# Kernel tuning notes

Measured on AMD Instinct MI355X. Metric: run time of the kernel, lower is better.

Reference implementation:

```python
import jax, jax.numpy as jnp
import numpy as np

N_NODES = 20000
N_EDGES = 8192
UNITS = 128
NUM_GAUSSIANS = 50
CUTOFF = 8.0
GAMMA = 10.0
MIN_DIST, MAX_DIST = 0.0, 30.0


def setup_inputs() -> dict:
    key = jax.random.key(0)
    ks = jax.random.split(key, 6)
    node_features = jax.random.normal(ks[0], (N_NODES, UNITS), dtype=jnp.float32)
    edge_indices = jax.random.randint(ks[1], (2, N_EDGES), 0, N_NODES, dtype=jnp.int32)
    distances = jax.random.uniform(ks[2], (N_EDGES,), dtype=jnp.float32)
    # filter network params (Dense(units) -> swish -> Dense(units*units))
    W1 = jax.random.normal(ks[3], (NUM_GAUSSIANS, UNITS), dtype=jnp.float32) / np.sqrt(NUM_GAUSSIANS)
    b1 = jnp.zeros((UNITS,), dtype=jnp.float32)
    W2 = jax.random.normal(ks[4], (UNITS, UNITS * UNITS), dtype=jnp.float32) / np.sqrt(UNITS)
    b2 = jnp.zeros((UNITS * UNITS,), dtype=jnp.float32)
    # transform Dense(units, use_bias=False)
    Wt = jax.random.normal(ks[5], (UNITS, UNITS), dtype=jnp.float32) / np.sqrt(UNITS)
    return {"node_features": node_features, "edge_indices": edge_indices,
            "distances": distances, "W1": W1, "b1": b1, "W2": W2, "b2": b2, "Wt": Wt}


def reference(node_features, edge_indices, distances, W1, b1, W2, b2, Wt):
    n_nodes, units = node_features.shape
    # cutoff mask (multiplicative; dropped edges contribute zero to the scatter-sum,
    # equivalent to tf.boolean_mask + unsorted_segment_sum)
    mask = (distances <= CUTOFF).astype(node_features.dtype)  # [E]
    # Gaussian basis expansion
    centers = jnp.linspace(MIN_DIST, MAX_DIST, NUM_GAUSSIANS, dtype=jnp.float32)
    df = jnp.exp(-GAMMA * jnp.square(distances[:, None] - centers[None, :]))  # [E, G]
    # filter network: Dense -> swish -> Dense(units*units)
    h = jax.nn.silu(df @ W1 + b1)                    # [E, U]
    filters = (h @ W2 + b2).reshape(-1, units, units)  # [E, U, U]
    # gather source node features, transform, per-edge matvec
    src = node_features[edge_indices[0]]             # [E, U]
    transformed = src @ Wt                           # [E, U]
    filtered = jnp.einsum('eij,ej->ei', filters, transformed) * mask[:, None]  # [E, U]
    # scatter-sum to destination nodes
    messages = jax.ops.segment_sum(filtered, edge_indices[1], num_segments=n_nodes)
    return jax.nn.silu(messages)
```

## Files before the change

kernel.cpp:

```cpp
#include <hip/hip_runtime.h>
#include <hip/hip_fp16.h>


typedef _Float16 f16;
typedef __attribute__((ext_vector_type(8))) f16 f16x8;
typedef __attribute__((ext_vector_type(4))) float f32x4;
typedef __attribute__((ext_vector_type(4))) unsigned int u32x4;

#define NEDGE 8192
#define NNODE 20000
#define NG    50
#define KSTEPS 516
#define W2C_BYTES (KSTEPS * 8192)
#define HT_BYTES (64 * 132 * 128 * 2)
#define TM_BYTES (NEDGE * 128 * 2)

#define LDS_H   0
#define LDS_TM  5120
#define LDS_TOT 37888

static __device__ __forceinline__ float fsilu(float x) { return x / (1.0f + __expf(-x)); }

static __device__ __forceinline__ void gll16(const void* g, void* l) {
  __builtin_amdgcn_global_load_lds(
      (const __attribute__((address_space(1))) unsigned int*)g,
      (__attribute__((address_space(3))) unsigned int*)l, 16, 0, 0);
}

__global__ __launch_bounds__(256) void k0_w2c(const float* __restrict__ W2,
                                              const float* __restrict__ b2,
                                              f16* __restrict__ w2c) {
  int gidx = blockIdx.x * 256 + threadIdx.x;
  int lane = gidx & 63;
  int nt   = (gidx >> 6) & 7;
  int step = gidx >> 9;
  int k0i = step * 32 + (lane >> 4) * 8;
  int i   = nt * 16 + (lane & 15);
  int u   = k0i >> 7, j0 = k0i & 127;
  const float* src = (u < 128) ? (W2 + (size_t)u * 16384 + i * 128 + j0)
                               : (b2 + i * 128 + j0);
  union { f16 s[8]; u32x4 v; } pk;
#pragma unroll
  for (int r = 0; r < 8; ++r) pk.s[r] = (f16)src[r];
  *((u32x4*)w2c + gidx) = pk.v;
}

__global__ __launch_bounds__(256) void k1_edge(const float* __restrict__ NF,
                                               const int*   __restrict__ EI,
                                               const float* __restrict__ DI,
                                               const float* __restrict__ W1,
                                               const float* __restrict__ B1,
                                               const float* __restrict__ WT,
                                               f16* __restrict__ ht2,
                                               f16* __restrict__ tmo) {
  __shared__ float df[16][NG];
  __shared__ float s_mask[16];
  __shared__ float s_src[16][128];
  __shared__ float t_tile[16][132];
  __shared__ float h_tile[16][132];
  int et = blockIdx.x, e0 = et * 16, tid = threadIdx.x;

  for (int idx = tid; idx < 16 * NG; idx += 256) {
    int e = idx / NG, g = idx - e * NG;
    float d = DI[e0 + e];
    float x = d - (float)g * (30.0f / 49.0f);
    df[e][g] = __expf(-10.0f * x * x);
  }
  if (tid < 16) s_mask[tid] = (DI[e0 + tid] <= 8.0f) ? 1.0f : 0.0f;
  for (int idx = tid; idx < 16 * 128; idx += 256) {
    int e = idx >> 7, u = idx & 127;
    s_src[e][u] = NF[(size_t)EI[e0 + e] * 128 + u];
  }
  __syncthreads();

  int j = tid & 127, es = tid >> 7;
  for (int e = es * 8; e < es * 8 + 8; ++e) {
    float acc = B1[j];
    for (int g = 0; g < NG; ++g) acc += df[e][g] * W1[g * 128 + j];
    h_tile[e][j] = fsilu(acc);
  }
  {
    float acc[8] = {0.f,0.f,0.f,0.f,0.f,0.f,0.f,0.f};
    for (int u = 0; u < 128; ++u) {
      float wv = WT[u * 128 + j];
#pragma unroll
      for (int e8 = 0; e8 < 8; ++e8) acc[e8] += s_src[es * 8 + e8][u] * wv;
    }
#pragma unroll
    for (int e8 = 0; e8 < 8; ++e8) t_tile[es * 8 + e8][j] = acc[e8];
  }
  __syncthreads();

  int eb = et >> 3, el0 = (et & 7) * 16;
  {
    int u = tid >> 1, hf = tid & 1;
    union { f16 s[8]; u32x4 v; } pk;
#pragma unroll
    for (int k = 0; k < 8; ++k) pk.s[k] = (f16)h_tile[hf * 8 + k][u];
    *(u32x4*)(ht2 + ((size_t)eb * 132 + u) * 128 + el0 + hf * 8) = pk.v;
  }
  if (tid < 16) ht2[((size_t)eb * 132 + 128) * 128 + el0 + tid] = (f16)1.0f;
  {
    int e = tid >> 4, cc = tid & 15;
    float m = s_mask[e];
    union { f16 s[8]; u32x4 v; } pk;
#pragma unroll
    for (int k = 0; k < 8; ++k) pk.s[k] = (f16)(m * t_tile[e][cc * 8 + k]);
    int col = (cc * 16) ^ ((e & 7) << 4);
    *(u32x4*)((char*)tmo + (size_t)(e0 + e) * 256 + col) = pk.v;
  }
}

__global__ __launch_bounds__(256, 2) void k2_gemm(const f16* __restrict__ w2c,
                                                  const f16* __restrict__ ht2,
                                                  const f16* __restrict__ tm,
                                                  const int* __restrict__ EI,
                                                  float* __restrict__ msg) {
  __shared__ u32x4 smem_v[LDS_TOT / 16];
  char* smem = (char*)smem_v;

  const int bid = blockIdx.x;
  const int c   = bid & 7;
  const int eb  = bid >> 3;
  const int e0  = eb * 128;
  const int nu  = (c == 7) ? 17 : 16;
  const int tid = threadIdx.x, w = tid >> 6, lane = tid & 63;
  const int l15 = lane & 15, g4 = lane >> 4;
  const int wm = w >> 1, wn = w & 1;

  {
    const char* tsrc = (const char*)tm + (size_t)e0 * 256 + w * 8192;
#pragma unroll
    for (int q = 0; q < 8; ++q)
      gll16(tsrc + q * 1024 + lane * 16,
            smem + LDS_TM + w * 8192 + q * 1024 + lane * 16);
  }
  if (w == 0) {
    const char* hsrc = (const char*)ht2 + ((size_t)eb * 132 + c * 16) * 256;
#pragma unroll
    for (int q = 0; q < 5; ++q)
      gll16(hsrc + q * 1024 + lane * 16, smem + LDS_H + q * 1024 + lane * 16);
  }
  __syncthreads();

  f16x8 Tall[4][4];
  {
    const int tmrow = LDS_TM + (wm * 64 + l15) * 256;
    const int colsw = (l15 & 7) << 4;
#pragma unroll
    for (int rt = 0; rt < 4; ++rt)
#pragma unroll
      for (int jc = 0; jc < 4; ++jc)
        Tall[rt][jc] = *(const f16x8*)(smem + tmrow + rt * 4096 +
                                       ((jc * 64 + g4 * 16) ^ colsw));
  }
  const __half* hbase = (const __half*)(smem + LDS_H) + wm * 64 + l15;

  __half2 hc[4], hn[4];
#pragma unroll
  for (int rt = 0; rt < 4; ++rt) hc[rt] = __half2half2(hbase[rt * 16]);

  const char* bp = (const char*)w2c + (size_t)(c * 64) * 8192 + wn * 4096 + lane * 16;
  f16x8 Bc[4], Bn[4];
#pragma unroll
  for (int nt = 0; nt < 4; ++nt) Bn[nt] = *(const f16x8*)(bp + nt * 1024);
  bp += 8192;

  f32x4 acc[4][4];
#pragma unroll
  for (int rt = 0; rt < 4; ++rt)
#pragma unroll
    for (int nt = 0; nt < 4; ++nt) acc[rt][nt] = (f32x4){0.f, 0.f, 0.f, 0.f};

  for (int u = 0; u < nu; ++u) {
#pragma unroll
    for (int jc = 0; jc < 4; ++jc) {
#pragma unroll
      for (int nt = 0; nt < 4; ++nt) Bc[nt] = Bn[nt];
#pragma unroll
      for (int nt = 0; nt < 4; ++nt) Bn[nt] = *(const f16x8*)(bp + nt * 1024);
      bp += 8192;
      if (jc == 1) {
#pragma unroll
        for (int rt = 0; rt < 4; ++rt)
          hn[rt] = __half2half2(hbase[(u + 1) * 128 + rt * 16]);
      }
      union uf { f16x8 v; __half2 h[4]; };
      uf a[4];
#pragma unroll
      for (int rt = 0; rt < 4; ++rt) {
        uf t; t.v = Tall[rt][jc];
#pragma unroll
        for (int q = 0; q < 4; ++q) a[rt].h[q] = __hmul2(t.h[q], hc[rt]);
      }
      __builtin_amdgcn_s_setprio(1);
#pragma unroll
      for (int nt = 0; nt < 4; ++nt)
#pragma unroll
        for (int rt = 0; rt < 4; ++rt)
          acc[rt][nt] = __builtin_amdgcn_mfma_f32_16x16x32_f16(a[rt].v, Bc[nt], acc[rt][nt], 0, 0, 0);
      __builtin_amdgcn_s_setprio(0);
    }
#pragma unroll
    for (int rt = 0; rt < 4; ++rt) hc[rt] = hn[rt];
  }

  const int* dst = EI + NEDGE;
#pragma unroll
  for (int rt = 0; rt < 4; ++rt) {
#pragma unroll
    for (int r = 0; r < 4; ++r) {
      int e = e0 + wm * 64 + rt * 16 + g4 * 4 + r;
      float* row = msg + (size_t)dst[e] * 128 + wn * 64 + l15;
#pragma unroll
      for (int nt = 0; nt < 4; ++nt)
        atomicAdd(row + nt * 16, acc[rt][nt][r]);
    }
  }
}

__global__ __launch_bounds__(256) void k3_silu(float* __restrict__ out, int n4) {
  int idx = blockIdx.x * 256 + threadIdx.x;
  int stride = gridDim.x * 256;
  f32x4* p = (f32x4*)out;
  for (; idx < n4; idx += stride) {
    f32x4 v = p[idx];
#pragma unroll
    for (int cc = 0; cc < 4; ++cc) v[cc] = fsilu(v[cc]);
    p[idx] = v;
  }
}

extern "C" void kernel_launch(void* const* d_in, const int* in_sizes, int n_in,
                              void* d_out, int out_size, void* d_ws, size_t ws_size,
                              hipStream_t stream) {
  const float* NF = (const float*)d_in[0];
  const int*   EI = (const int*)  d_in[1];
  const float* DI = (const float*)d_in[2];
  const float* W1 = (const float*)d_in[3];
  const float* B1 = (const float*)d_in[4];
  const float* W2 = (const float*)d_in[5];
  const float* B2 = (const float*)d_in[6];
  const float* WT = (const float*)d_in[7];
  float* out = (float*)d_out;

  f16* w2c = (f16*)d_ws;
  f16* ht2 = (f16*)((char*)d_ws + W2C_BYTES);
  f16* tmo = (f16*)((char*)d_ws + W2C_BYTES + HT_BYTES);
  size_t needed = (size_t)W2C_BYTES + HT_BYTES + TM_BYTES;
  if (ws_size < needed) return;

  hipMemsetAsync(d_out, 0, (size_t)out_size * sizeof(float), stream);
  k0_w2c <<<dim3(1032), dim3(256), 0, stream>>>(W2, B2, w2c);
  k1_edge<<<dim3(512),  dim3(256), 0, stream>>>(NF, EI, DI, W1, B1, WT, ht2, tmo);
  k2_gemm<<<dim3(512),  dim3(256), 0, stream>>>(w2c, ht2, tmo, EI, out);
  k3_silu<<<dim3(1024), dim3(256), 0, stream>>>(out, out_size / 4);
}
```

Baseline: 89.63 us.

## Fuse weight conversion, edge prep and zeroing; split GEMM across eight waves

The W2 f16 conversion, the per-edge filter and transform prep, and the output zeroing now run as block ranges of one kernel, replacing three separate launches including a memset. The edge GEMM kernel moves from 256 to 512 threads, so each wave owns 32 edge rows instead of 64. This halves the per-wave accumulator and A-operand registers and raises the number of resident waves. In exchange, each W2 B-fragment is now fetched from global memory by twice as many waves, which adds cache traffic.

Result: slower. 91.99 us (+2.6%).

```diff
diff --git a/kernel.cpp b/kernel.cpp
--- a/kernel.cpp
+++ b/kernel.cpp
@@ -27,91 +27,106 @@
       (__attribute__((address_space(3))) unsigned int*)l, 16, 0, 0);
 }
 
-__global__ __launch_bounds__(256) void k0_w2c(const float* __restrict__ W2,
-                                              const float* __restrict__ b2,
-                                              f16* __restrict__ w2c) {
-  int gidx = blockIdx.x * 256 + threadIdx.x;
-  int lane = gidx & 63;
-  int nt   = (gidx >> 6) & 7;
-  int step = gidx >> 9;
-  int k0i = step * 32 + (lane >> 4) * 8;
-  int i   = nt * 16 + (lane & 15);
-  int u   = k0i >> 7, j0 = k0i & 127;
-  const float* src = (u < 128) ? (W2 + (size_t)u * 16384 + i * 128 + j0)
-                               : (b2 + i * 128 + j0);
-  union { f16 s[8]; u32x4 v; } pk;
-#pragma unroll
-  for (int r = 0; r < 8; ++r) pk.s[r] = (f16)src[r];
-  *((u32x4*)w2c + gidx) = pk.v;
-}
-
-__global__ __launch_bounds__(256) void k1_edge(const float* __restrict__ NF,
-                                               const int*   __restrict__ EI,
-                                               const float* __restrict__ DI,
-                                               const float* __restrict__ W1,
-                                               const float* __restrict__ B1,
-                                               const float* __restrict__ WT,
-                                               f16* __restrict__ ht2,
-                                               f16* __restrict__ tmo) {
+__global__ __launch_bounds__(256) void k01(const float* __restrict__ W2,
+                                           const float* __restrict__ b2,
+                                           const float* __restrict__ NF,
+                                           const int*   __restrict__ EI,
+                                           const float* __restrict__ DI,
+                                           const float* __restrict__ W1,
+                                           const float* __restrict__ B1,
+                                           const float* __restrict__ WT,
+                                           f16* __restrict__ w2c,
+                                           f16* __restrict__ ht2,
+                                           f16* __restrict__ tmo,
+                                           float* __restrict__ out, int nz4) {
   __shared__ float df[16][NG];
   __shared__ float s_mask[16];
   __shared__ float s_src[16][128];
   __shared__ float t_tile[16][132];
   __shared__ float h_tile[16][132];
-  int et = blockIdx.x, e0 = et * 16, tid = threadIdx.x;
-
-  for (int idx = tid; idx < 16 * NG; idx += 256) {
-    int e = idx / NG, g = idx - e * NG;
-    float d = DI[e0 + e];
-    float x = d - (float)g * (30.0f / 49.0f);
-    df[e][g] = __expf(-10.0f * x * x);
-  }
-  if (tid < 16) s_mask[tid] = (DI[e0 + tid] <= 8.0f) ? 1.0f : 0.0f;
-  for (int idx = tid; idx < 16 * 128; idx += 256) {
-    int e = idx >> 7, u = idx & 127;
-    s_src[e][u] = NF[(size_t)EI[e0 + e] * 128 + u];
-  }
-  __syncthreads();
-
-  int j = tid & 127, es = tid >> 7;
-  for (int e = es * 8; e < es * 8 + 8; ++e) {
-    float acc = B1[j];
-    for (int g = 0; g < NG; ++g) acc += df[e][g] * W1[g * 128 + j];
-    h_tile[e][j] = fsilu(acc);
+  const int bid = blockIdx.x, tid = threadIdx.x;
+
+  if (bid < 1032) {
+    int gidx = bid * 256 + tid;
+    int lane = gidx & 63;
+    int nt   = (gidx >> 6) & 7;
+    int step = gidx >> 9;
+    int k0i = step * 32 + (lane >> 4) * 8;
+    int i   = nt * 16 + (lane & 15);
+    int u   = k0i >> 7, j0 = k0i & 127;
+    const float* src = (u < 128) ? (W2 + (size_t)u * 16384 + i * 128 + j0)
+                                 : (b2 + i * 128 + j0);
+    union { f16 s[8]; u32x4 v; } pk;
+#pragma unroll
+    for (int r = 0; r < 8; ++r) pk.s[r] = (f16)src[r];
+    *((u32x4*)w2c + gidx) = pk.v;
+    return;
+  }
+  if (bid < 1544) {
+    int et = bid - 1032, e0 = et * 16;
+    for (int idx = tid; idx < 16 * NG; idx += 256) {
+      int e = idx / NG, g = idx - e * NG;
+      float d = DI[e0 + e];
+      float x = d - (float)g * (30.0f / 49.0f);
+      df[e][g] = __expf(-10.0f * x * x);
+    }
+    if (tid < 16) s_mask[tid] = (DI[e0 + tid] <= 8.0f) ? 1.0f : 0.0f;
+    for (int idx = tid; idx < 16 * 128; idx += 256) {
+      int e = idx >> 7, u = idx & 127;
+      s_src[e][u] = NF[(size_t)EI[e0 + e] * 128 + u];
+    }
+    __syncthreads();
+
+    int j = tid & 127, es = tid >> 7;
+    for (int e = es * 8; e < es * 8 + 8; ++e) {
+      float acc = B1[j];
+      for (int g = 0; g < NG; ++g) acc += df[e][g] * W1[g * 128 + j];
+      h_tile[e][j] = fsilu(acc);
+    }
+    {
+      float acc[8] = {0.f,0.f,0.f,0.f,0.f,0.f,0.f,0.f};
+      for (int u = 0; u < 128; ++u) {
+        float wv = WT[u * 128 + j];
+#pragma unroll
+        for (int e8 = 0; e8 < 8; ++e8) acc[e8] += s_src[es * 8 + e8][u] * wv;
+      }
+#pragma unroll
+      for (int e8 = 0; e8 < 8; ++e8) t_tile[es * 8 + e8][j] = acc[e8];
+    }
+    __syncthreads();
+
+    int eb = et >> 3, el0 = (et & 7) * 16;
+    {
+      int u = tid >> 1, hf = tid & 1;
+      union { f16 s[8]; u32x4 v; } pk;
+#pragma unroll
+      for (int k = 0; k < 8; ++k) pk.s[k] = (f16)h_tile[hf * 8 + k][u];
+      *(u32x4*)(ht2 + ((size_t)eb * 132 + u) * 128 + el0 + hf * 8) = pk.v;
+    }
+    if (tid < 16) ht2[((size_t)eb * 132 + 128) * 128 + el0 + tid] = (f16)1.0f;
+    {
+      int e = tid >> 4, cc = tid & 15;
+      float m = s_mask[e];
+      union { f16 s[8]; u32x4 v; } pk;
+#pragma unroll
+      for (int k = 0; k < 8; ++k) pk.s[k] = (f16)(m * t_tile[e][cc * 8 + k]);
+      int col = (cc * 16) ^ ((e & 7) << 4);
+      *(u32x4*)((char*)tmo + (size_t)(e0 + e) * 256 + col) = pk.v;
+    }
+    return;
   }
   {
-    float acc[8] = {0.f,0.f,0.f,0.f,0.f,0.f,0.f,0.f};
-    for (int u = 0; u < 128; ++u) {
-      float wv = WT[u * 128 + j];
-#pragma unroll
-      for (int e8 = 0; e8 < 8; ++e8) acc[e8] += s_src[es * 8 + e8][u] * wv;
-    }
-#pragma unroll
-    for (int e8 = 0; e8 < 8; ++e8) t_tile[es * 8 + e8][j] = acc[e8];
-  }
-  __syncthreads();
-
-  int eb = et >> 3, el0 = (et & 7) * 16;
-  {
-    int u = tid >> 1, hf = tid & 1;
-    union { f16 s[8]; u32x4 v; } pk;
-#pragma unroll
-    for (int k = 0; k < 8; ++k) pk.s[k] = (f16)h_tile[hf * 8 + k][u];
-    *(u32x4*)(ht2 + ((size_t)eb * 132 + u) * 128 + el0 + hf * 8) = pk.v;
-  }
-  if (tid < 16) ht2[((size_t)eb * 132 + 128) * 128 + el0 + tid] = (f16)1.0f;
-  {
-    int e = tid >> 4, cc = tid & 15;
-    float m = s_mask[e];
-    union { f16 s[8]; u32x4 v; } pk;
-#pragma unroll
-    for (int k = 0; k < 8; ++k) pk.s[k] = (f16)(m * t_tile[e][cc * 8 + k]);
-    int col = (cc * 16) ^ ((e & 7) << 4);
-    *(u32x4*)((char*)tmo + (size_t)(e0 + e) * 256 + col) = pk.v;
-  }
-}
-
-__global__ __launch_bounds__(256, 2) void k2_gemm(const f16* __restrict__ w2c,
+    int base = (bid - 1544) * 1024;
+    f32x4 z = {0.f, 0.f, 0.f, 0.f};
+#pragma unroll
+    for (int k = 0; k < 4; ++k) {
+      int i4 = base + k * 256 + tid;
+      if (i4 < nz4) ((f32x4*)out)[i4] = z;
+    }
+  }
+}
+
+__global__ __launch_bounds__(512, 4) void k2_gemm(const f16* __restrict__ w2c,
                                                   const f16* __restrict__ ht2,
                                                   const f16* __restrict__ tm,
                                                   const int* __restrict__ EI,
@@ -129,36 +144,35 @@
   const int wm = w >> 1, wn = w & 1;
 
   {
-    const char* tsrc = (const char*)tm + (size_t)e0 * 256 + w * 8192;
-#pragma unroll
-    for (int q = 0; q < 8; ++q)
-      gll16(tsrc + q * 1024 + lane * 16,
-            smem + LDS_TM + w * 8192 + q * 1024 + lane * 16);
-  }
-  if (w == 0) {
+    const char* tsrc = (const char*)tm + (size_t)e0 * 256;
+#pragma unroll
+    for (int q = 0; q < 4; ++q) {
+      int off = (q * 512 + tid) * 16;
+      gll16(tsrc + off, smem + LDS_TM + off);
+    }
+  }
+  if (tid < 320) {
     const char* hsrc = (const char*)ht2 + ((size_t)eb * 132 + c * 16) * 256;
-#pragma unroll
-    for (int q = 0; q < 5; ++q)
-      gll16(hsrc + q * 1024 + lane * 16, smem + LDS_H + q * 1024 + lane * 16);
+    gll16(hsrc + tid * 16, smem + LDS_H + tid * 16);
   }
   __syncthreads();
 
-  f16x8 Tall[4][4];
+  f16x8 Tall[2][4];
   {
-    const int tmrow = LDS_TM + (wm * 64 + l15) * 256;
+    const int tmrow = LDS_TM + (wm * 32 + l15) * 256;
     const int colsw = (l15 & 7) << 4;
 #pragma unroll
-    for (int rt = 0; rt < 4; ++rt)
+    for (int rt = 0; rt < 2; ++rt)
 #pragma unroll
       for (int jc = 0; jc < 4; ++jc)
         Tall[rt][jc] = *(const f16x8*)(smem + tmrow + rt * 4096 +
                                        ((jc * 64 + g4 * 16) ^ colsw));
   }
-  const __half* hbase = (const __half*)(smem + LDS_H) + wm * 64 + l15;
-
-  __half2 hc[4], hn[4];
-#pragma unroll
-  for (int rt = 0; rt < 4; ++rt) hc[rt] = __half2half2(hbase[rt * 16]);
+  const __half* hbase = (const __half*)(smem + LDS_H) + wm * 32 + l15;
+
+  __half2 hc[2], hn[2];
+#pragma unroll
+  for (int rt = 0; rt < 2; ++rt) hc[rt] = __half2half2(hbase[rt * 16]);
 
   const char* bp = (const char*)w2c + (size_t)(c * 64) * 8192 + wn * 4096 + lane * 16;
   f16x8 Bc[4], Bn[4];
@@ -166,9 +180,9 @@
   for (int nt = 0; nt < 4; ++nt) Bn[nt] = *(const f16x8*)(bp + nt * 1024);
   bp += 8192;
 
-  f32x4 acc[4][4];
-#pragma unroll
-  for (int rt = 0; rt < 4; ++rt)
+  f32x4 acc[2][4];
+#pragma unroll
+  for (int rt = 0; rt < 2; ++rt)
 #pragma unroll
     for (int nt = 0; nt < 4; ++nt) acc[rt][nt] = (f32x4){0.f, 0.f, 0.f, 0.f};
 
@@ -182,13 +196,13 @@
       bp += 8192;
       if (jc == 1) {
 #pragma unroll
-        for (int rt = 0; rt < 4; ++rt)
+        for (int rt = 0; rt < 2; ++rt)
           hn[rt] = __half2half2(hbase[(u + 1) * 128 + rt * 16]);
       }
       union uf { f16x8 v; __half2 h[4]; };
-      uf a[4];
-#pragma unroll
-      for (int rt = 0; rt < 4; ++rt) {
+      uf a[2];
+#pragma unroll
+      for (int rt = 0; rt < 2; ++rt) {
         uf t; t.v = Tall[rt][jc];
 #pragma unroll
         for (int q = 0; q < 4; ++q) a[rt].h[q] = __hmul2(t.h[q], hc[rt]);
@@ -197,20 +211,20 @@
 #pragma unroll
       for (int nt = 0; nt < 4; ++nt)
 #pragma unroll
-        for (int rt = 0; rt < 4; ++rt)
+        for (int rt = 0; rt < 2; ++rt)
           acc[rt][nt] = __builtin_amdgcn_mfma_f32_16x16x32_f16(a[rt].v, Bc[nt], acc[rt][nt], 0, 0, 0);
       __builtin_amdgcn_s_setprio(0);
     }
 #pragma unroll
-    for (int rt = 0; rt < 4; ++rt) hc[rt] = hn[rt];
+    for (int rt = 0; rt < 2; ++rt) hc[rt] = hn[rt];
   }
 
   const int* dst = EI + NEDGE;
 #pragma unroll
-  for (int rt = 0; rt < 4; ++rt) {
+  for (int rt = 0; rt < 2; ++rt) {
 #pragma unroll
     for (int r = 0; r < 4; ++r) {
-      int e = e0 + wm * 64 + rt * 16 + g4 * 4 + r;
+      int e = e0 + wm * 32 + rt * 16 + g4 * 4 + r;
       float* row = msg + (size_t)dst[e] * 128 + wn * 64 + l15;
 #pragma unroll
       for (int nt = 0; nt < 4; ++nt)
@@ -250,9 +264,10 @@
   size_t needed = (size_t)W2C_BYTES + HT_BYTES + TM_BYTES;
   if (ws_size < needed) return;
 
-  hipMemsetAsync(d_out, 0, (size_t)out_size * sizeof(float), stream);
-  k0_w2c <<<dim3(1032), dim3(256), 0, stream>>>(W2, B2, w2c);
-  k1_edge<<<dim3(512),  dim3(256), 0, stream>>>(NF, EI, DI, W1, B1, WT, ht2, tmo);
-  k2_gemm<<<dim3(512),  dim3(256), 0, stream>>>(w2c, ht2, tmo, EI, out);
-  k3_silu<<<dim3(1024), dim3(256), 0, stream>>>(out, out_size / 4);
-}
+  int nz4 = out_size / 4;
+  int zb  = (nz4 + 1023) / 1024;
+  k01    <<<dim3(1544 + zb), dim3(256), 0, stream>>>(W2, B2, NF, EI, DI, W1, B1, WT,
+                                                     w2c, ht2, tmo, out, nz4);
+  k2_gemm<<<dim3(512),       dim3(512), 0, stream>>>(w2c, ht2, tmo, EI, out);
+  k3_silu<<<dim3(1024),      dim3(256), 0, stream>>>(out, out_size / 4);
+}
```

## Merge memset, W2 conversion and edge prep into one launch; double-buffer B loads

Applied to the files above, without the earlier changes.

Combines the output memset, the W2-to-fp16 repacking kernel and the per-edge feature kernel into a single launch whose blocks branch on block index, removing two launches and the serialization between them. The GEMM inner loop now uses two alternating B register buffers, and each nt slice is reloaded right after its MFMAs with a clamped offset, replacing the copy-then-load prefetch. This aims to cut launch and inter-kernel gaps and give loads more latency cover, at the cost of higher register pressure and a mixed-role kernel whose branches diverge in LDS and resource usage.

Result: no change. 88.42 us (-1.3%).

```diff
diff --git a/kernel.cpp b/kernel.cpp
--- a/kernel.cpp
+++ b/kernel.cpp
@@ -27,87 +27,102 @@
       (__attribute__((address_space(3))) unsigned int*)l, 16, 0, 0);
 }
 
-__global__ __launch_bounds__(256) void k0_w2c(const float* __restrict__ W2,
-                                              const float* __restrict__ b2,
-                                              f16* __restrict__ w2c) {
-  int gidx = blockIdx.x * 256 + threadIdx.x;
-  int lane = gidx & 63;
-  int nt   = (gidx >> 6) & 7;
-  int step = gidx >> 9;
-  int k0i = step * 32 + (lane >> 4) * 8;
-  int i   = nt * 16 + (lane & 15);
-  int u   = k0i >> 7, j0 = k0i & 127;
-  const float* src = (u < 128) ? (W2 + (size_t)u * 16384 + i * 128 + j0)
-                               : (b2 + i * 128 + j0);
-  union { f16 s[8]; u32x4 v; } pk;
-#pragma unroll
-  for (int r = 0; r < 8; ++r) pk.s[r] = (f16)src[r];
-  *((u32x4*)w2c + gidx) = pk.v;
-}
-
-__global__ __launch_bounds__(256) void k1_edge(const float* __restrict__ NF,
-                                               const int*   __restrict__ EI,
-                                               const float* __restrict__ DI,
-                                               const float* __restrict__ W1,
-                                               const float* __restrict__ B1,
-                                               const float* __restrict__ WT,
-                                               f16* __restrict__ ht2,
-                                               f16* __restrict__ tmo) {
+__global__ __launch_bounds__(256) void k01(const float* __restrict__ W2,
+                                           const float* __restrict__ b2,
+                                           const float* __restrict__ NF,
+                                           const int*   __restrict__ EI,
+                                           const float* __restrict__ DI,
+                                           const float* __restrict__ W1,
+                                           const float* __restrict__ B1,
+                                           const float* __restrict__ WT,
+                                           f16* __restrict__ w2c,
+                                           f16* __restrict__ ht2,
+                                           f16* __restrict__ tmo,
+                                           float* __restrict__ out, int nz4) {
   __shared__ float df[16][NG];
   __shared__ float s_mask[16];
   __shared__ float s_src[16][128];
   __shared__ float t_tile[16][132];
   __shared__ float h_tile[16][132];
-  int et = blockIdx.x, e0 = et * 16, tid = threadIdx.x;
-
-  for (int idx = tid; idx < 16 * NG; idx += 256) {
-    int e = idx / NG, g = idx - e * NG;
-    float d = DI[e0 + e];
-    float x = d - (float)g * (30.0f / 49.0f);
-    df[e][g] = __expf(-10.0f * x * x);
-  }
-  if (tid < 16) s_mask[tid] = (DI[e0 + tid] <= 8.0f) ? 1.0f : 0.0f;
-  for (int idx = tid; idx < 16 * 128; idx += 256) {
-    int e = idx >> 7, u = idx & 127;
-    s_src[e][u] = NF[(size_t)EI[e0 + e] * 128 + u];
-  }
-  __syncthreads();
-
-  int j = tid & 127, es = tid >> 7;
-  for (int e = es * 8; e < es * 8 + 8; ++e) {
-    float acc = B1[j];
-    for (int g = 0; g < NG; ++g) acc += df[e][g] * W1[g * 128 + j];
-    h_tile[e][j] = fsilu(acc);
+  const int bid = blockIdx.x, tid = threadIdx.x;
+
+  if (bid < 1032) {
+    int gidx = bid * 256 + tid;
+    int lane = gidx & 63;
+    int nt   = (gidx >> 6) & 7;
+    int step = gidx >> 9;
+    int k0i = step * 32 + (lane >> 4) * 8;
+    int i   = nt * 16 + (lane & 15);
+    int u   = k0i >> 7, j0 = k0i & 127;
+    const float* src = (u < 128) ? (W2 + (size_t)u * 16384 + i * 128 + j0)
+                                 : (b2 + i * 128 + j0);
+    union { f16 s[8]; u32x4 v; } pk;
+#pragma unroll
+    for (int r = 0; r < 8; ++r) pk.s[r] = (f16)src[r];
+    *((u32x4*)w2c + gidx) = pk.v;
+    return;
+  }
+  if (bid < 1544) {
+    int et = bid - 1032, e0 = et * 16;
+    for (int idx = tid; idx < 16 * NG; idx += 256) {
+      int e = idx / NG, g = idx - e * NG;
+      float d = DI[e0 + e];
+      float x = d - (float)g * (30.0f / 49.0f);
+      df[e][g] = __expf(-10.0f * x * x);
+    }
+    if (tid < 16) s_mask[tid] = (DI[e0 + tid] <= 8.0f) ? 1.0f : 0.0f;
+    for (int idx = tid; idx < 16 * 128; idx += 256) {
+      int e = idx >> 7, u = idx & 127;
+      s_src[e][u] = NF[(size_t)EI[e0 + e] * 128 + u];
+    }
+    __syncthreads();
+
+    int j = tid & 127, es = tid >> 7;
+    for (int e = es * 8; e < es * 8 + 8; ++e) {
+      float acc = B1[j];
+      for (int g = 0; g < NG; ++g) acc += df[e][g] * W1[g * 128 + j];
+      h_tile[e][j] = fsilu(acc);
+    }
+    {
+      float acc[8] = {0.f,0.f,0.f,0.f,0.f,0.f,0.f,0.f};
+      for (int u = 0; u < 128; ++u) {
+        float wv = WT[u * 128 + j];
+#pragma unroll
+        for (int e8 = 0; e8 < 8; ++e8) acc[e8] += s_src[es * 8 + e8][u] * wv;
+      }
+#pragma unroll
+      for (int e8 = 0; e8 < 8; ++e8) t_tile[es * 8 + e8][j] = acc[e8];
+    }
+    __syncthreads();
+
+    int eb = et >> 3, el0 = (et & 7) * 16;
+    {
+      int u = tid >> 1, hf = tid & 1;
+      union { f16 s[8]; u32x4 v; } pk;
+#pragma unroll
+      for (int k = 0; k < 8; ++k) pk.s[k] = (f16)h_tile[hf * 8 + k][u];
+      *(u32x4*)(ht2 + ((size_t)eb * 132 + u) * 128 + el0 + hf * 8) = pk.v;
+    }
+    if (tid < 16) ht2[((size_t)eb * 132 + 128) * 128 + el0 + tid] = (f16)1.0f;
+    {
+      int e = tid >> 4, cc = tid & 15;
+      float m = s_mask[e];
+      union { f16 s[8]; u32x4 v; } pk;
+#pragma unroll
+      for (int k = 0; k < 8; ++k) pk.s[k] = (f16)(m * t_tile[e][cc * 8 + k]);
+      int col = (cc * 16) ^ ((e & 7) << 4);
+      *(u32x4*)((char*)tmo + (size_t)(e0 + e) * 256 + col) = pk.v;
+    }
+    return;
   }
   {
-    float acc[8] = {0.f,0.f,0.f,0.f,0.f,0.f,0.f,0.f};
-    for (int u = 0; u < 128; ++u) {
-      float wv = WT[u * 128 + j];
-#pragma unroll
-      for (int e8 = 0; e8 < 8; ++e8) acc[e8] += s_src[es * 8 + e8][u] * wv;
-    }
-#pragma unroll
-    for (int e8 = 0; e8 < 8; ++e8) t_tile[es * 8 + e8][j] = acc[e8];
-  }
-  __syncthreads();
-
-  int eb = et >> 3, el0 = (et & 7) * 16;
-  {
-    int u = tid >> 1, hf = tid & 1;
-    union { f16 s[8]; u32x4 v; } pk;
-#pragma unroll
-    for (int k = 0; k < 8; ++k) pk.s[k] = (f16)h_tile[hf * 8 + k][u];
-    *(u32x4*)(ht2 + ((size_t)eb * 132 + u) * 128 + el0 + hf * 8) = pk.v;
-  }
-  if (tid < 16) ht2[((size_t)eb * 132 + 128) * 128 + el0 + tid] = (f16)1.0f;
-  {
-    int e = tid >> 4, cc = tid & 15;
-    float m = s_mask[e];
-    union { f16 s[8]; u32x4 v; } pk;
-#pragma unroll
-    for (int k = 0; k < 8; ++k) pk.s[k] = (f16)(m * t_tile[e][cc * 8 + k]);
-    int col = (cc * 16) ^ ((e & 7) << 4);
-    *(u32x4*)((char*)tmo + (size_t)(e0 + e) * 256 + col) = pk.v;
+    int base = (bid - 1544) * 1024;
+    f32x4 z = {0.f, 0.f, 0.f, 0.f};
+#pragma unroll
+    for (int k = 0; k < 4; ++k) {
+      int i4 = base + k * 256 + tid;
+      if (i4 < nz4) ((f32x4*)out)[i4] = z;
+    }
   }
 }
 
@@ -161,10 +176,13 @@
   for (int rt = 0; rt < 4; ++rt) hc[rt] = __half2half2(hbase[rt * 16]);
 
   const char* bp = (const char*)w2c + (size_t)(c * 64) * 8192 + wn * 4096 + lane * 16;
-  f16x8 Bc[4], Bn[4];
-#pragma unroll
-  for (int nt = 0; nt < 4; ++nt) Bn[nt] = *(const f16x8*)(bp + nt * 1024);
-  bp += 8192;
+  const size_t offmax = (size_t)(nu * 4 - 1) * 8192;
+  f16x8 B0[4], B1[4];
+#pragma unroll
+  for (int nt = 0; nt < 4; ++nt) B0[nt] = *(const f16x8*)(bp + nt * 1024);
+#pragma unroll
+  for (int nt = 0; nt < 4; ++nt) B1[nt] = *(const f16x8*)(bp + 8192 + nt * 1024);
+  size_t off = 2 * 8192;
 
   f32x4 acc[4][4];
 #pragma unroll
@@ -175,11 +193,6 @@
   for (int u = 0; u < nu; ++u) {
 #pragma unroll
     for (int jc = 0; jc < 4; ++jc) {
-#pragma unroll
-      for (int nt = 0; nt < 4; ++nt) Bc[nt] = Bn[nt];
-#pragma unroll
-      for (int nt = 0; nt < 4; ++nt) Bn[nt] = *(const f16x8*)(bp + nt * 1024);
-      bp += 8192;
       if (jc == 1) {
 #pragma unroll
         for (int rt = 0; rt < 4; ++rt)
@@ -193,13 +206,24 @@
 #pragma unroll
         for (int q = 0; q < 4; ++q) a[rt].h[q] = __hmul2(t.h[q], hc[rt]);
       }
+      size_t o = off; if (o > offmax) o = offmax;
       __builtin_amdgcn_s_setprio(1);
 #pragma unroll
-      for (int nt = 0; nt < 4; ++nt)
-#pragma unroll
-        for (int rt = 0; rt < 4; ++rt)
-          acc[rt][nt] = __builtin_amdgcn_mfma_f32_16x16x32_f16(a[rt].v, Bc[nt], acc[rt][nt], 0, 0, 0);
+      for (int nt = 0; nt < 4; ++nt) {
+        if ((jc & 1) == 0) {
+#pragma unroll
+          for (int rt = 0; rt < 4; ++rt)
+            acc[rt][nt] = __builtin_amdgcn_mfma_f32_16x16x32_f16(a[rt].v, B0[nt], acc[rt][nt], 0, 0, 0);
+          B0[nt] = *(const f16x8*)(bp + o + nt * 1024);
+        } else {
+#pragma unroll
+          for (int rt = 0; rt < 4; ++rt)
+            acc[rt][nt] = __builtin_amdgcn_mfma_f32_16x16x32_f16(a[rt].v, B1[nt], acc[rt][nt], 0, 0, 0);
+          B1[nt] = *(const f16x8*)(bp + o + nt * 1024);
+        }
+      }
       __builtin_amdgcn_s_setprio(0);
+      off += 8192;
     }
 #pragma unroll
     for (int rt = 0; rt < 4; ++rt) hc[rt] = hn[rt];
@@ -250,9 +274,10 @@
   size_t needed = (size_t)W2C_BYTES + HT_BYTES + TM_BYTES;
   if (ws_size < needed) return;
 
-  hipMemsetAsync(d_out, 0, (size_t)out_size * sizeof(float), stream);
-  k0_w2c <<<dim3(1032), dim3(256), 0, stream>>>(W2, B2, w2c);
-  k1_edge<<<dim3(512),  dim3(256), 0, stream>>>(NF, EI, DI, W1, B1, WT, ht2, tmo);
-  k2_gemm<<<dim3(512),  dim3(256), 0, stream>>>(w2c, ht2, tmo, EI, out);
-  k3_silu<<<dim3(1024), dim3(256), 0, stream>>>(out, out_size / 4);
-}
+  int nz4 = out_size / 4;
+  int zb  = (nz4 + 1023) / 1024;
+  k01    <<<dim3(1544 + zb), dim3(256), 0, stream>>>(W2, B2, NF, EI, DI, W1, B1, WT,
+                                                     w2c, ht2, tmo, out, nz4);
+  k2_gemm<<<dim3(512),       dim3(256), 0, stream>>>(w2c, ht2, tmo, EI, out);
+  k3_silu<<<dim3(1024),      dim3(256), 0, stream>>>(out, out_size / 4);
+}
```
